# Optimization experiments

Hardware: AMD Instinct MI355X
Metric: run time of the kernel (lower is better)

## Reference

```python
import jax, jax.numpy as jnp
import numpy as np

EPS = 1e-6

def setup_inputs() -> dict:
    key = jax.random.key(0)
    k1, k2, k3 = jax.random.split(key, 3)
    B, D, T = 4096, 4096, 16
    inputs = jax.random.normal(k1, (B, D), dtype=jnp.float32)
    W = jax.random.normal(k2, (D, T), dtype=jnp.float32)
    W_static = jax.random.normal(k3, (D, T), dtype=jnp.float32)
    return {"inputs": inputs, "W": W, "W_static": W_static}


def _znorm(A):
    # batch z-normalization per column (population std, matching tf.math.reduce_std)
    return (A - A.mean(axis=0)) / (A.std(axis=0) + EPS)


def _pls_scan(X, Ws):
    """Sequential PLS-style deflation: factor i is produced after
    orthogonalizing X against the z-normalized previous factors."""
    B = X.shape[0]
    denom = jnp.asarray(B, X.dtype)
    T = Ws.shape[1]
    cols = [X @ Ws[:, 0:1]]  # [B,1]
    for i in range(1, T):
        C = jnp.concatenate(cols, axis=1)          # [B,i]
        conv = _znorm(C)                           # [B,i]
        beta = (conv.T @ X) / denom                # [i,D]
        lin = X - conv @ beta                      # deflated inputs [B,D]
        cols.append(lin @ Ws[:, i:i + 1])
    return jnp.concatenate(cols, axis=1)           # [B,T]


def reference(inputs, W, W_static):
    # training path of FactorLayer.call
    X = _znorm(inputs)                              # batchnorm of inputs [B,D]
    c_mat = _pls_scan(X, W_static)                  # calculate_cmat with static weights
    B = X.shape[0]
    denom = jnp.asarray(B, X.dtype)
    T = W.shape[1]
    outs = [X @ W[:, 0:1]]
    for i in range(1, T):
        Cs = c_mat[:, :i]
        conv = _znorm(Cs)
        beta = (conv.T @ X) / denom                 # [i,D]
        lin = X - conv @ beta                       # training_run output [B,D]
        outs.append(lin @ W[:, i:i + 1])
    return jnp.concatenate(outs, axis=1)            # [B,T]
```

## Files before the change

kernel.cpp:

```cpp
#include <hip/hip_runtime.h>
#include <stdint.h>


#define BB 4096
#define DD 4096
#define EPSF 1e-6f

#define O_PART    0u
#define O_WSF     1048576u
#define O_GRAMM   1179648u
#define O_YZ      1188608u
#define O_YPART   1319680u

__device__ __forceinline__ int gidx(int a, int b) {
    int lo = a < b ? a : b, hi = a < b ? b : a;
    return lo * 33 + hi;
}

__global__ __launch_bounds__(256, 2)
void kA(const float* __restrict__ in, float* __restrict__ ws) {
    int b = blockIdx.x, t = threadIdx.x;
    int idx = b * 256 + t;
    if (idx < 8960) ws[O_GRAMM + idx] = 0.f;
    int cgk = b & 3, rg = b >> 2;
    int c0 = cgk * 1024 + t * 4, r0 = rg * 32;
    float s0=0.f,s1=0.f,s2=0.f,s3=0.f,q0=0.f,q1=0.f,q2=0.f,q3=0.f;
    #pragma unroll 4
    for (int r = 0; r < 32; ++r) {
        float4 u = *(const float4*)&in[(size_t)(r0 + r) * DD + c0];
        s0 += u.x; q0 += u.x*u.x;  s1 += u.y; q1 += u.y*u.y;
        s2 += u.z; q2 += u.z*u.z;  s3 += u.w; q3 += u.w*u.w;
    }
    float* part = ws + O_PART + (size_t)rg * 8192;
    *(float4*)&part[c0]        = make_float4(s0, s1, s2, s3);
    *(float4*)&part[4096 + c0] = make_float4(q0, q1, q2, q3);
}

__global__ __launch_bounds__(256, 4)
void kD(const float* __restrict__ W, const float* __restrict__ Wstat,
        float* __restrict__ ws) {
    __shared__ float red[32][9], redq[32][9], invs[32];
    int b = blockIdx.x, t = threadIdx.x;
    int dbase = b * 32;
    {
        int c1 = t & 31, k1 = t >> 5;
        const float* part = ws + O_PART;
        float s = 0.f, q = 0.f;
        #pragma unroll
        for (int i = 0; i < 16; ++i) {
            int g = k1 * 16 + i;
            s += part[(size_t)g * 8192 + dbase + c1];
            q += part[(size_t)g * 8192 + 4096 + dbase + c1];
        }
        red[c1][k1] = s; redq[c1][k1] = q;
    }
    __syncthreads();
    if (t < 32) {
        float ss = 0.f, qq = 0.f;
        #pragma unroll
        for (int i = 0; i < 8; ++i) { ss += red[t][i]; qq += redq[t][i]; }
        float m = ss * (1.0f / BB);
        float var = qq * (1.0f / BB) - m * m; if (var < 0.f) var = 0.f;
        invs[t] = 1.0f / (sqrtf(var) + EPSF);
    }
    __syncthreads();
    {
        int c2 = t >> 3, j0 = (t & 7) * 4;
        int d = dbase + c2;
        float iv = invs[c2];
        float4 wv = (j0 < 16) ? *(const float4*)&Wstat[d * 16 + j0]
                              : *(const float4*)&W[d * 16 + (j0 - 16)];
        *(float4*)&ws[O_WSF + (size_t)d * 32 + j0] =
            make_float4(wv.x * iv, wv.y * iv, wv.z * iv, wv.w * iv);
    }
}

__global__ __launch_bounds__(256, 8)
void kB(const float* __restrict__ in, const float* __restrict__ ws,
        float* __restrict__ ypart) {
    __shared__ __align__(16) float tile[64 * 33];
    int b = blockIdx.x, t = threadIdx.x;
    int dg = b & 31, rg = b >> 5;
    int dbase = dg * 128, rowbase = rg * 64;
    float acc[8];
    #pragma unroll
    for (int i = 0; i < 8; ++i) acc[i] = 0.f;
    int chunk = t & 7, srow = t >> 3;
    int row = t & 63;
    int jq = __builtin_amdgcn_readfirstlane(t >> 6);
    const float* wsf = ws + O_WSF;
    const float* inp = in + (size_t)(rowbase + srow) * DD + dbase + chunk * 4;
    float4 pf0 = *(const float4*)(inp);
    float4 pf1 = *(const float4*)(inp + (size_t)32 * DD);
    for (int stage = 0; stage < 4; ++stage) {
        int ds0 = stage * 32;
        int b0 = srow * 33 + chunk * 4;
        tile[b0 + 0] = pf0.x; tile[b0 + 1] = pf0.y;
        tile[b0 + 2] = pf0.z; tile[b0 + 3] = pf0.w;
        int b1 = (srow + 32) * 33 + chunk * 4;
        tile[b1 + 0] = pf1.x; tile[b1 + 1] = pf1.y;
        tile[b1 + 2] = pf1.z; tile[b1 + 3] = pf1.w;
        __syncthreads();
        if (stage < 3) {
            pf0 = *(const float4*)(inp + (stage + 1) * 32);
            pf1 = *(const float4*)(inp + (size_t)32 * DD + (stage + 1) * 32);
        }
        const float* trow = tile + row * 33;
        #pragma unroll 4
        for (int dl = 0; dl < 32; ++dl) {
            float xs = trow[dl];
            const float* wr = wsf + (size_t)(dbase + ds0 + dl) * 32 + jq * 8;
            #pragma unroll
            for (int j = 0; j < 8; ++j) acc[j] += xs * wr[j];
        }
        __syncthreads();
    }
    float* dst = ypart + ((size_t)dg * BB + rowbase + row) * 32 + jq * 8;
    *(float4*)(dst + 0) = make_float4(acc[0], acc[1], acc[2], acc[3]);
    *(float4*)(dst + 4) = make_float4(acc[4], acc[5], acc[6], acc[7]);
}

__global__ __launch_bounds__(256, 2)
void kC(float* __restrict__ ws) {
    __shared__ float yz_s[8 * 34];
    int b = blockIdx.x, t = threadIdx.x;
    int rowbase = b * 8;
    int r = t >> 5, c = t & 31;
    const float* yp = ws + O_YPART;
    size_t off = (size_t)(rowbase + r) * 32 + c;
    float s = 0.f;
    #pragma unroll
    for (int dg = 0; dg < 32; ++dg) s += yp[(size_t)dg * (BB * 32) + off];
    ws[O_YZ + off] = s;
    yz_s[r * 34 + c] = s;
    if (c == 0) yz_s[r * 34 + 32] = 1.0f;
    __syncthreads();
    float* gm = ws + O_GRAMM + (size_t)(b & 7) * 1120;
    for (int p = t; p < 561; p += 256) {
        int i = 0, rem = p;
        while (rem >= 33 - i) { rem -= 33 - i; ++i; }
        int j = i + rem;
        float a2 = 0.f;
        #pragma unroll
        for (int r2 = 0; r2 < 8; ++r2) a2 += yz_s[r2 * 34 + i] * yz_s[r2 * 34 + j];
        atomicAdd(&gm[i * 33 + j], a2);
    }
}

__global__ __launch_bounds__(256, 2)
void kE(const float* __restrict__ ws, float* __restrict__ out) {
    __shared__ __align__(16) float yzs[64 * 36];
    __shared__ float Sv[33], GA[17 * 17], gz[17 * 16], v[15][17], gad[15][16],
                     gzd[15][16], gu[17], u[17], st[2], wm[17 * 16];
    int b = blockIdx.x, t = threadIdx.x;
    int rowbase = b * 64;
    const float invB = 1.0f / BB;
    const float4* src = (const float4*)(ws + O_YZ) + (size_t)rowbase * 8;
    #pragma unroll
    for (int k = 0; k < 2; ++k) {
        int idx = k * 256 + t;
        float4 f = src[idx];
        int row = idx >> 3, c4 = (idx & 7) * 4;
        yzs[row * 36 + c4 + 0] = f.x; yzs[row * 36 + c4 + 1] = f.y;
        yzs[row * 36 + c4 + 2] = f.z; yzs[row * 36 + c4 + 3] = f.w;
    }
    const float* gm = ws + O_GRAMM;
    if (t < 33) {
        float s = 0.f;
        #pragma unroll
        for (int m = 0; m < 8; ++m) s += gm[m * 1120 + gidx(t, 32)];
        Sv[t] = s;
    }
    __syncthreads();
    for (int idx = t; idx < 17 * 17; idx += 256) {
        int p = idx / 17, q = idx % 17;
        float val;
        if (p < 16 && q < 16) {
            float raw = 0.f;
            #pragma unroll
            for (int m = 0; m < 8; ++m) raw += gm[m * 1120 + gidx(p, q)];
            val = raw - Sv[p] * Sv[q] * invB;
        } else if (p == 16 && q == 16) val = (float)BB;
        else val = 0.f;
        GA[idx] = val;
    }
    for (int idx = t; idx < 17 * 16; idx += 256) {
        int p = idx / 16, tt = idx % 16;
        float val = 0.f;
        if (p < 16) {
            float raw = 0.f;
            #pragma unroll
            for (int m = 0; m < 8; ++m) raw += gm[m * 1120 + gidx(p, 16 + tt)];
            val = raw - Sv[p] * Sv[16 + tt] * invB;
        }
        gz[idx] = val;
    }
    if (t < 17) u[t] = (t == 0) ? 1.f : 0.f;
    __syncthreads();
    for (int i = 0; i < 15; ++i) {
        if (t < 17) {
            float s = 0.f;
            for (int q = 0; q < 17; ++q) s += GA[t * 17 + q] * u[q];
            gu[t] = s;
        }
        __syncthreads();
        if (t == 0) {
            float mean = gu[16] * invB, e2 = 0.f;
            for (int p = 0; p < 17; ++p) e2 += u[p] * gu[p];
            e2 *= invB;
            float var = e2 - mean * mean; if (var < 0.f) var = 0.f;
            st[0] = mean; st[1] = 1.0f / (sqrtf(var) + EPSF);
        }
        __syncthreads();
        if (t < 17) v[i][t] = (u[t] - (t == 16 ? st[0] : 0.f)) * st[1];
        __syncthreads();
        if (t < 16) {
            float s = 0.f;
            for (int p = 0; p < 17; ++p) s += v[i][p] * GA[p * 17 + t];
            gad[i][t] = s;
        } else if (t < 32) {
            int tt = t - 16;
            float s = 0.f;
            for (int p = 0; p < 17; ++p) s += v[i][p] * gz[p * 16 + tt];
            gzd[i][tt] = s;
        }
        __syncthreads();
        if (t < 17) {
            float a2 = 0.f;
            for (int j = 0; j <= i; ++j) a2 += v[j][t] * gad[j][i + 1];
            u[t] = ((t == i + 1) ? 1.f : 0.f) - a2 * invB;
        }
        __syncthreads();
    }
    for (int idx = t; idx < 17 * 16; idx += 256) {
        int p = idx / 16, tt = idx % 16;
        float s = 0.f;
        for (int j = 0; j < tt; ++j) s += v[j][p] * gzd[j][tt];
        wm[idx] = s * invB;
    }
    __syncthreads();
    if (t < 16) {
        float adj = Sv[16 + t] * invB;
        for (int p = 0; p < 16; ++p) adj -= Sv[p] * invB * wm[p * 16 + t];
        wm[16 * 16 + t] += adj;
    }
    __syncthreads();
    int row = t >> 2, c0 = (t & 3) * 4;
    const float* yr = yzs + row * 36;
    float o[4];
    #pragma unroll
    for (int k = 0; k < 4; ++k) o[k] = yr[16 + c0 + k] - wm[16 * 16 + c0 + k];
    #pragma unroll
    for (int p = 0; p < 16; ++p) {
        float yp = yr[p];
        #pragma unroll
        for (int k = 0; k < 4; ++k) o[k] -= yp * wm[p * 16 + c0 + k];
    }
    *(float4*)&out[(size_t)rowbase * 16 + t * 4] = make_float4(o[0], o[1], o[2], o[3]);
}

extern "C" void kernel_launch(void* const* d_in, const int* in_sizes, int n_in,
                              void* d_out, int out_size, void* d_ws, size_t ws_size,
                              hipStream_t stream) {
    const float* in    = (const float*)d_in[0];
    const float* W     = (const float*)d_in[1];
    const float* Wstat = (const float*)d_in[2];
    float* ws  = (float*)d_ws;
    float* out = (float*)d_out;

    kA<<<dim3(512),  dim3(256), 0, stream>>>(in, ws);
    kD<<<dim3(128),  dim3(256), 0, stream>>>(W, Wstat, ws);
    kB<<<dim3(2048), dim3(256), 0, stream>>>(in, ws, ws + O_YPART);
    kC<<<dim3(512),  dim3(256), 0, stream>>>(ws);
    kE<<<dim3(64),   dim3(256), 0, stream>>>(ws, out);
}
```

Baseline: 151.6 us.

## Fuse per-column inverse-std scaling into the projection kernel and drop kD

Removes the separate kD launch that pre-scaled W and W_static by each column's inverse std. Instead, every kB block reduces the 16 partial sums for its 128 columns, computes inv-std in shared memory, and scales the input tile before multiplying by the raw weights. kA is reorganised so each block covers 256 rows by 128 columns and reduces through shared memory, giving 16 partial groups instead of 128. This saves one launch and the workspace round trip for the scaled weights. In exchange, each of the 2048 kB blocks repeats the partial-sum reduction and adds a sync.

```diff
diff --git a/kernel.cpp b/kernel.cpp
--- a/kernel.cpp
+++ b/kernel.cpp
@@ -7,10 +7,9 @@
 #define EPSF 1e-6f
 
 #define O_PART    0u
-#define O_WSF     1048576u
-#define O_GRAMM   1179648u
-#define O_YZ      1188608u
-#define O_YPART   1319680u
+#define O_GRAMM   131072u
+#define O_YZ      140288u
+#define O_YPART   271360u
 
 __device__ __forceinline__ int gidx(int a, int b) {
     int lo = a < b ? a : b, hi = a < b ? b : a;
@@ -19,87 +18,84 @@
 
 __global__ __launch_bounds__(256, 2)
 void kA(const float* __restrict__ in, float* __restrict__ ws) {
+    __shared__ float rs[8 * 132], rq[8 * 132];
     int b = blockIdx.x, t = threadIdx.x;
     int idx = b * 256 + t;
     if (idx < 8960) ws[O_GRAMM + idx] = 0.f;
-    int cgk = b & 3, rg = b >> 2;
-    int c0 = cgk * 1024 + t * 4, r0 = rg * 32;
+    int cg = b & 31, rg = b >> 5;
+    int dbase = cg * 128, r0 = rg * 256;
+    int chunk = t & 31, rr = t >> 5;
+    int c0 = dbase + chunk * 4;
     float s0=0.f,s1=0.f,s2=0.f,s3=0.f,q0=0.f,q1=0.f,q2=0.f,q3=0.f;
     #pragma unroll 4
-    for (int r = 0; r < 32; ++r) {
-        float4 u = *(const float4*)&in[(size_t)(r0 + r) * DD + c0];
+    for (int i = 0; i < 32; ++i) {
+        int r = r0 + i * 8 + rr;
+        float4 u = *(const float4*)&in[(size_t)r * DD + c0];
         s0 += u.x; q0 += u.x*u.x;  s1 += u.y; q1 += u.y*u.y;
         s2 += u.z; q2 += u.z*u.z;  s3 += u.w; q3 += u.w*u.w;
     }
+    int lb = rr * 132 + chunk * 4;
+    rs[lb+0]=s0; rs[lb+1]=s1; rs[lb+2]=s2; rs[lb+3]=s3;
+    rq[lb+0]=q0; rq[lb+1]=q1; rq[lb+2]=q2; rq[lb+3]=q3;
+    __syncthreads();
     float* part = ws + O_PART + (size_t)rg * 8192;
-    *(float4*)&part[c0]        = make_float4(s0, s1, s2, s3);
-    *(float4*)&part[4096 + c0] = make_float4(q0, q1, q2, q3);
-}
-
-__global__ __launch_bounds__(256, 4)
-void kD(const float* __restrict__ W, const float* __restrict__ Wstat,
-        float* __restrict__ ws) {
-    __shared__ float red[32][9], redq[32][9], invs[32];
-    int b = blockIdx.x, t = threadIdx.x;
-    int dbase = b * 32;
-    {
-        int c1 = t & 31, k1 = t >> 5;
-        const float* part = ws + O_PART;
-        float s = 0.f, q = 0.f;
-        #pragma unroll
-        for (int i = 0; i < 16; ++i) {
-            int g = k1 * 16 + i;
-            s += part[(size_t)g * 8192 + dbase + c1];
-            q += part[(size_t)g * 8192 + 4096 + dbase + c1];
-        }
-        red[c1][k1] = s; redq[c1][k1] = q;
-    }
-    __syncthreads();
-    if (t < 32) {
-        float ss = 0.f, qq = 0.f;
-        #pragma unroll
-        for (int i = 0; i < 8; ++i) { ss += red[t][i]; qq += redq[t][i]; }
-        float m = ss * (1.0f / BB);
-        float var = qq * (1.0f / BB) - m * m; if (var < 0.f) var = 0.f;
-        invs[t] = 1.0f / (sqrtf(var) + EPSF);
-    }
-    __syncthreads();
-    {
-        int c2 = t >> 3, j0 = (t & 7) * 4;
-        int d = dbase + c2;
-        float iv = invs[c2];
-        float4 wv = (j0 < 16) ? *(const float4*)&Wstat[d * 16 + j0]
-                              : *(const float4*)&W[d * 16 + (j0 - 16)];
-        *(float4*)&ws[O_WSF + (size_t)d * 32 + j0] =
-            make_float4(wv.x * iv, wv.y * iv, wv.z * iv, wv.w * iv);
+    if (t < 128) {
+        float a = 0.f;
+        #pragma unroll
+        for (int r2 = 0; r2 < 8; ++r2) a += rs[r2 * 132 + t];
+        part[dbase + t] = a;
+    } else {
+        int ci = t - 128;
+        float a = 0.f;
+        #pragma unroll
+        for (int r2 = 0; r2 < 8; ++r2) a += rq[r2 * 132 + ci];
+        part[4096 + dbase + ci] = a;
     }
 }
 
 __global__ __launch_bounds__(256, 8)
-void kB(const float* __restrict__ in, const float* __restrict__ ws,
+void kB(const float* __restrict__ in, const float* __restrict__ W,
+        const float* __restrict__ Wstat, float* __restrict__ ws,
         float* __restrict__ ypart) {
     __shared__ __align__(16) float tile[64 * 33];
+    __shared__ __align__(16) float inv_s[128];
     int b = blockIdx.x, t = threadIdx.x;
     int dg = b & 31, rg = b >> 5;
     int dbase = dg * 128, rowbase = rg * 64;
-    float acc[8];
-    #pragma unroll
-    for (int i = 0; i < 8; ++i) acc[i] = 0.f;
     int chunk = t & 7, srow = t >> 3;
     int row = t & 63;
     int jq = __builtin_amdgcn_readfirstlane(t >> 6);
-    const float* wsf = ws + O_WSF;
     const float* inp = in + (size_t)(rowbase + srow) * DD + dbase + chunk * 4;
     float4 pf0 = *(const float4*)(inp);
     float4 pf1 = *(const float4*)(inp + (size_t)32 * DD);
+    {
+        if (t < 128) {
+            const float* part = ws + O_PART;
+            float s = 0.f, q = 0.f;
+            #pragma unroll
+            for (int g = 0; g < 16; ++g) {
+                s += part[(size_t)g * 8192 + dbase + t];
+                q += part[(size_t)g * 8192 + 4096 + dbase + t];
+            }
+            float m = s * (1.0f / BB);
+            float var = q * (1.0f / BB) - m * m; if (var < 0.f) var = 0.f;
+            inv_s[t] = 1.0f / (sqrtf(var) + EPSF);
+        }
+        __syncthreads();
+    }
+    float acc[8];
+    #pragma unroll
+    for (int i = 0; i < 8; ++i) acc[i] = 0.f;
+    const float* wbase = (jq < 2) ? (Wstat + jq * 8) : (W + (jq - 2) * 8);
     for (int stage = 0; stage < 4; ++stage) {
         int ds0 = stage * 32;
+        float4 iv4 = *(const float4*)&inv_s[ds0 + chunk * 4];
         int b0 = srow * 33 + chunk * 4;
-        tile[b0 + 0] = pf0.x; tile[b0 + 1] = pf0.y;
-        tile[b0 + 2] = pf0.z; tile[b0 + 3] = pf0.w;
+        tile[b0 + 0] = pf0.x * iv4.x; tile[b0 + 1] = pf0.y * iv4.y;
+        tile[b0 + 2] = pf0.z * iv4.z; tile[b0 + 3] = pf0.w * iv4.w;
         int b1 = (srow + 32) * 33 + chunk * 4;
-        tile[b1 + 0] = pf1.x; tile[b1 + 1] = pf1.y;
-        tile[b1 + 2] = pf1.z; tile[b1 + 3] = pf1.w;
+        tile[b1 + 0] = pf1.x * iv4.x; tile[b1 + 1] = pf1.y * iv4.y;
+        tile[b1 + 2] = pf1.z * iv4.z; tile[b1 + 3] = pf1.w * iv4.w;
         __syncthreads();
         if (stage < 3) {
             pf0 = *(const float4*)(inp + (stage + 1) * 32);
@@ -109,7 +105,7 @@
         #pragma unroll 4
         for (int dl = 0; dl < 32; ++dl) {
             float xs = trow[dl];
-            const float* wr = wsf + (size_t)(dbase + ds0 + dl) * 32 + jq * 8;
+            const float* wr = wbase + (size_t)(dbase + ds0 + dl) * 16;
             #pragma unroll
             for (int j = 0; j < 8; ++j) acc[j] += xs * wr[j];
         }
@@ -269,8 +265,7 @@
     float* out = (float*)d_out;
 
     kA<<<dim3(512),  dim3(256), 0, stream>>>(in, ws);
-    kD<<<dim3(128),  dim3(256), 0, stream>>>(W, Wstat, ws);
-    kB<<<dim3(2048), dim3(256), 0, stream>>>(in, ws, ws + O_YPART);
+    kB<<<dim3(2048), dim3(256), 0, stream>>>(in, W, Wstat, ws, ws + O_YPART);
     kC<<<dim3(512),  dim3(256), 0, stream>>>(ws);
     kE<<<dim3(64),   dim3(256), 0, stream>>>(ws, out);
 }
```

Result: no change. 149.1 us (-1.6%).
